# Optimization experiments

Measured on AMD Instinct MI355X. Metric: run time of the kernel, lower is better.

The kernel has to match this reference:

```python
import jax, jax.numpy as jnp
import numpy as np

N = 100000
E = 800000


def sage_conv(h, src, dst, W_l, W_r, b):
    # PyG SAGEConv (mean aggr): lin_l(mean_{j in N(i)} h_j) + lin_r(h_i) + bias
    deg = jax.ops.segment_sum(jnp.ones((src.shape[0],), h.dtype), dst, num_segments=N)
    agg = jax.ops.segment_sum(h[src], dst, num_segments=N)  # [N, d]
    agg = agg / jnp.maximum(deg, 1.0)[:, None]
    return agg @ W_l + h @ W_r + b


def gcn_conv(h, src, dst, W, b):
    # PyG GCNConv with added self-loops and symmetric normalization
    xw = h @ W  # [N, out]
    deg = jax.ops.segment_sum(jnp.ones((src.shape[0],), h.dtype), dst, num_segments=N) + 1.0
    dinv = jax.lax.rsqrt(deg)
    coef = dinv[src] * dinv[dst]  # [E]
    out = jax.ops.segment_sum(xw[src] * coef[:, None], dst, num_segments=N)
    out = out + xw * (1.0 / deg)[:, None]  # self-loop term: dinv[i]*dinv[i]
    return out + b


def fit_and_add(x, h):
    # initial_residual: zero-pad x along feature dim to h's width, then add
    d_in, d_out = x.shape[1], h.shape[1]
    if d_in < d_out:
        x = jnp.pad(x, ((0, 0), (0, d_out - d_in)))
    return x + h


def setup_inputs() -> dict:
    key = jax.random.key(0)
    ks = jax.random.split(key, 12)
    s = lambda d: 1.0 / np.sqrt(d)
    x = jax.random.normal(ks[0], (N, 128), jnp.float32)
    edge_index = jax.random.randint(ks[1], (2, E), 0, N, jnp.int32)
    return {
        "x": x,
        "edge_index": edge_index,
        "W1_l": jax.random.normal(ks[2], (128, 256), jnp.float32) * s(128),
        "W1_r": jax.random.normal(ks[3], (128, 256), jnp.float32) * s(128),
        "b1": jnp.zeros((256,), jnp.float32),
        "W2_l": jax.random.normal(ks[4], (256, 256), jnp.float32) * s(256),
        "W2_r": jax.random.normal(ks[5], (256, 256), jnp.float32) * s(256),
        "b2": jnp.zeros((256,), jnp.float32),
        "Wr": jax.random.normal(ks[6], (128, 256), jnp.float32) * s(128),
        "br": jnp.zeros((256,), jnp.float32),
        "Wmu": jax.random.normal(ks[7], (256, 64), jnp.float32) * s(256),
        "bmu": jnp.zeros((64,), jnp.float32),
        "Wls": jax.random.normal(ks[8], (256, 64), jnp.float32) * s(256),
        "bls": jnp.zeros((64,), jnp.float32),
    }


def reference(x, edge_index, W1_l, W1_r, b1, W2_l, W2_r, b2, Wr, br, Wmu, bmu, Wls, bls):
    src, dst = edge_index[0], edge_index[1]
    h = jax.nn.relu(sage_conv(x, src, dst, W1_l, W1_r, b1))
    h = fit_and_add(x, h)
    h = jax.nn.relu(sage_conv(h, src, dst, W2_l, W2_r, b2))
    h = h + (x @ Wr + br)
    mu = gcn_conv(h, src, dst, Wmu, bmu)
    logstd = gcn_conv(h, src, dst, Wls, bls)
    return mu, logstd
```

## Files before the change

### kernel.cpp

```cpp
#include <hip/hip_runtime.h>
#include <hip/hip_bf16.h>

#define NN 100000
#define EE 800000
#define MPAD 100096
#define MT64 1564
#define MT128 782

typedef __attribute__((ext_vector_type(4))) float f32x4;
typedef __attribute__((ext_vector_type(8))) short s16x8;

__device__ __forceinline__ float bfu(unsigned short u) {
    union { unsigned i; float f; } x; x.i = ((unsigned)u) << 16; return x.f;
}
__device__ __forceinline__ unsigned short fbf(float f) {
    union { float f; unsigned i; } x; x.f = f;
    unsigned r = x.i + (((x.i >> 16) & 1u) + 0x7fffu);
    return (unsigned short)(r >> 16);
}
__device__ __forceinline__ uint4 pack8(const float* a) {
    uint4 o;
    o.x = (unsigned)fbf(a[0]) | ((unsigned)fbf(a[1]) << 16);
    o.y = (unsigned)fbf(a[2]) | ((unsigned)fbf(a[3]) << 16);
    o.z = (unsigned)fbf(a[4]) | ((unsigned)fbf(a[5]) << 16);
    o.w = (unsigned)fbf(a[6]) | ((unsigned)fbf(a[7]) << 16);
    return o;
}
__device__ __forceinline__ void acc8(float* a, uint4 v) {
    a[0] += bfu((unsigned short)v.x); a[1] += bfu((unsigned short)(v.x >> 16));
    a[2] += bfu((unsigned short)v.y); a[3] += bfu((unsigned short)(v.y >> 16));
    a[4] += bfu((unsigned short)v.z); a[5] += bfu((unsigned short)(v.z >> 16));
    a[6] += bfu((unsigned short)v.w); a[7] += bfu((unsigned short)(v.w >> 16));
}
__device__ __forceinline__ void load_lds16(const void* g, void* l) {
    __builtin_amdgcn_global_load_lds((const __attribute__((address_space(1))) void*)g,
                                     (__attribute__((address_space(3))) void*)l, 16, 0, 0);
}


__global__ void hist_k(const int* __restrict__ ei, int* __restrict__ counts) {
    int e = blockIdx.x * 256 + threadIdx.x;
    if (e < EE) atomicAdd(&counts[ei[EE + e]], 1);
}

__global__ void scan1_k(const int* __restrict__ counts, int* __restrict__ rp, int* __restrict__ bsum) {
    __shared__ int lds[256];
    int b = blockIdx.x, t = threadIdx.x;
    int base = b * 1024 + t * 4;
    int v[4]; int s = 0;
#pragma unroll
    for (int j = 0; j < 4; ++j) { v[j] = (base + j < NN) ? counts[base + j] : 0; s += v[j]; }
    lds[t] = s; __syncthreads();
    for (int off = 1; off < 256; off <<= 1) {
        int x = (t >= off) ? lds[t - off] : 0;
        __syncthreads();
        lds[t] += x;
        __syncthreads();
    }
    int run = lds[t] - s;
    if (t == 255) bsum[b] = lds[255];
#pragma unroll
    for (int j = 0; j < 4; ++j) { if (base + j < NN) rp[base + j] = run; run += v[j]; }
}

__global__ void scan2_k(int* __restrict__ bsum, int nb) {
    int l = threadIdx.x;
    int v0 = (l < nb) ? bsum[l] : 0;
    int v1 = (64 + l < nb) ? bsum[64 + l] : 0;
    int s0 = v0, s1 = v1;
    for (int off = 1; off < 64; off <<= 1) {
        int t0 = __shfl_up(s0, off); if (l >= off) s0 += t0;
        int t1 = __shfl_up(s1, off); if (l >= off) s1 += t1;
    }
    int tot0 = __shfl(s0, 63);
    if (l < nb) bsum[l] = s0 - v0;
    if (64 + l < nb) bsum[64 + l] = tot0 + s1 - v1;
}

__global__ void scan3_k(int* __restrict__ rp, const int* __restrict__ bsum,
                        int* __restrict__ counts, float* __restrict__ dinv) {
    int i = blockIdx.x * 256 + threadIdx.x;
    if (i == 0) rp[NN] = EE;
    if (i < NN) {
        int v = rp[i] + bsum[i >> 10];
        int deg = counts[i];
        rp[i] = v;
        counts[i] = v;
        dinv[i] = rsqrtf((float)deg + 1.0f);
    }
}

__global__ void fill_k(const int* __restrict__ ei, int* __restrict__ fill, int* __restrict__ esrc) {
    int e = blockIdx.x * 256 + threadIdx.x;
    if (e < EE) {
        int d = ei[EE + e];
        int slot = atomicAdd(&fill[d], 1);
        esrc[slot] = ei[e];
    }
}


__global__ void xcvt_k(const float* __restrict__ x, __hip_bfloat16* __restrict__ A1) {
    int idx = blockIdx.x * 256 + threadIdx.x;
    if (idx < NN * 32) {
        int row = idx >> 5; int c4 = (idx & 31) * 4;
        float4 v = *(const float4*)(x + (size_t)row * 128 + c4);
        ushort4 o; o.x = fbf(v.x); o.y = fbf(v.y); o.z = fbf(v.z); o.w = fbf(v.w);
        *(ushort4*)((unsigned short*)A1 + (size_t)row * 256 + 128 + c4) = o;
    }
}

__global__ void wprep_k(const float* __restrict__ W1l, const float* __restrict__ W1r,
                        const float* __restrict__ W2l, const float* __restrict__ W2r,
                        const float* __restrict__ Wr,  const float* __restrict__ Wmu,
                        const float* __restrict__ Wls,
                        unsigned short* __restrict__ B1T, unsigned short* __restrict__ B2T,
                        unsigned short* __restrict__ B3T) {
    int idx = blockIdx.x * 256 + threadIdx.x;
    if (idx < 65536) {
        int n = idx >> 8, k = idx & 255;
        float v = (k < 128) ? W1l[k * 256 + n] : W1r[(k - 128) * 256 + n];
        B1T[idx] = fbf(v);
    } else if (idx < 229376) {
        int j = idx - 65536;
        int n = j / 640, k = j - n * 640;
        float v = (k < 256) ? W2l[k * 256 + n]
                : (k < 512) ? W2r[(k - 256) * 256 + n]
                            : Wr[(k - 512) * 256 + n];
        B2T[j] = fbf(v);
    } else if (idx < 262144) {
        int j = idx - 229376;
        int n = j >> 8, k = j & 255;
        float v = (n < 64) ? Wmu[k * 64 + n] : Wls[k * 64 + (n - 64)];
        B3T[j] = fbf(v);
    }
}


__global__ __launch_bounds__(256) void agg1_k(const int* __restrict__ rp, const int* __restrict__ esrc,
                                              __hip_bfloat16* __restrict__ A1) {
    int wid = threadIdx.x >> 6, lane = threadIdx.x & 63;
    int node = blockIdx.x * 4 + wid;
    if (node >= NN) return;
    int e0 = rp[node], e1 = rp[node + 1];
    int sg = lane >> 4, lc = lane & 15;
    const unsigned short* X = (const unsigned short*)A1;
    float a[8] = {};
    for (int e = e0 + sg; e < e1; e += 4) {
        int s = esrc[e];
        uint4 v = *(const uint4*)(X + (size_t)s * 256 + 128 + lc * 8);
        acc8(a, v);
    }
#pragma unroll
    for (int k = 0; k < 8; ++k) {
        a[k] += __shfl_xor(a[k], 16);
        a[k] += __shfl_xor(a[k], 32);
    }
    int deg = e1 - e0;
    float sc = 1.0f / (float)(deg > 1 ? deg : 1);
    if (lane < 16) {
#pragma unroll
        for (int k = 0; k < 8; ++k) a[k] *= sc;
        *(uint4*)((unsigned short*)A1 + (size_t)node * 256 + lane * 8) = pack8(a);
    }
}

__global__ __launch_bounds__(256) void agg2_k(const int* __restrict__ rp, const int* __restrict__ esrc,
                                              const __hip_bfloat16* __restrict__ H1,
                                              __hip_bfloat16* __restrict__ AGG2) {
    int wid = threadIdx.x >> 6, lane = threadIdx.x & 63;
    int node = blockIdx.x * 4 + wid;
    if (node >= NN) return;
    int e0 = rp[node], e1 = rp[node + 1];
    int sg = lane >> 5, lc = lane & 31;
    const unsigned short* H = (const unsigned short*)H1;
    float a[8] = {};
    for (int e = e0 + sg; e < e1; e += 2) {
        int s = esrc[e];
        uint4 v = *(const uint4*)(H + (size_t)s * 256 + lc * 8);
        acc8(a, v);
    }
#pragma unroll
    for (int k = 0; k < 8; ++k) a[k] += __shfl_xor(a[k], 32);
    int deg = e1 - e0;
    float sc = 1.0f / (float)(deg > 1 ? deg : 1);
    if (lane < 32) {
#pragma unroll
        for (int k = 0; k < 8; ++k) a[k] *= sc;
        *(uint4*)((unsigned short*)AGG2 + (size_t)node * 256 + lane * 8) = pack8(a);
    }
}

__global__ __launch_bounds__(256) void gcnagg_k(const int* __restrict__ rp, const int* __restrict__ esrc,
                                                const __hip_bfloat16* __restrict__ XWS,
                                                const float* __restrict__ dinv,
                                                const float* __restrict__ bmu, const float* __restrict__ bls,
                                                float* __restrict__ out) {
    int wid = threadIdx.x >> 6, lane = threadIdx.x & 63;
    int node = blockIdx.x * 4 + wid;
    if (node >= NN) return;
    int e0 = rp[node], e1 = rp[node + 1];
    int sg = lane >> 4, lc = lane & 15;
    const unsigned short* W = (const unsigned short*)XWS;
    float a[8] = {};
    if (sg == 0) {
        uint4 v = *(const uint4*)(W + (size_t)node * 128 + lc * 8);
        acc8(a, v);
    }
    for (int e = e0 + sg; e < e1; e += 4) {
        int s = esrc[e];
        uint4 v = *(const uint4*)(W + (size_t)s * 128 + lc * 8);
        acc8(a, v);
    }
#pragma unroll
    for (int k = 0; k < 8; ++k) {
        a[k] += __shfl_xor(a[k], 16);
        a[k] += __shfl_xor(a[k], 32);
    }
    if (lane < 16) {
        float di = dinv[node];
        int col = lane * 8;
        float o[8];
        if (col < 64) {
#pragma unroll
            for (int k = 0; k < 8; ++k) o[k] = di * a[k] + bmu[col + k];
            *(float4*)(out + (size_t)node * 64 + col) = make_float4(o[0], o[1], o[2], o[3]);
            *(float4*)(out + (size_t)node * 64 + col + 4) = make_float4(o[4], o[5], o[6], o[7]);
        } else {
#pragma unroll
            for (int k = 0; k < 8; ++k) o[k] = di * a[k] + bls[col - 64 + k];
            *(float4*)(out + (size_t)NN * 64 + (size_t)node * 64 + (col - 64)) = make_float4(o[0], o[1], o[2], o[3]);
            *(float4*)(out + (size_t)NN * 64 + (size_t)node * 64 + (col - 60)) = make_float4(o[4], o[5], o[6], o[7]);
        }
    }
}


#define STAGE_T(SRC, LDST, STRIDE, ROWBASE, KOFF, NCH)                                              \
    _Pragma("unroll")                                                                               \
    for (int c_ = 0; c_ < NCH; ++c_) {                                                              \
        int off_ = (c_ * 256 + t) * 16;                                                             \
        int row_ = off_ >> 7;                                                                       \
        int cc_  = (off_ >> 4) & 7;                                                                 \
        int gcb_ = ((cc_ ^ (row_ & 7)) << 4);                                                       \
        int wb_ = (c_ * 256 + (t & ~63)) * 16;                                                      \
        load_lds16((const char*)(SRC) + ((size_t)((ROWBASE) + row_) * (STRIDE) + (KOFF)) * 2 + gcb_,\
                   (char*)(LDST) + wb_);                                                            \
    }

#define COMPUTE_STEP(ACC)                                                                          \
    _Pragma("unroll")                                                                              \
    for (int ks = 0; ks < 2; ++ks) {                                                               \
        int sc_ = (((ks << 2) + (lane >> 4)) ^ (lane & 7)) << 3;                                   \
        s16x8 afr[4], bfr[4];                                                                      \
        _Pragma("unroll")                                                                          \
        for (int i = 0; i < 4; ++i) {                                                              \
            afr[i] = *(const s16x8*)&lA[(wr * 64 + i * 16 + (lane & 15)) * 64 + sc_];              \
            bfr[i] = *(const s16x8*)&lB[(wc * 64 + i * 16 + (lane & 15)) * 64 + sc_];              \
        }                                                                                          \
        _Pragma("unroll")                                                                          \
        for (int i = 0; i < 4; ++i)                                                                \
            _Pragma("unroll")                                                                      \
            for (int j = 0; j < 4; ++j)                                                            \
                ACC[i][j] = __builtin_amdgcn_mfma_f32_16x16x32_bf16(afr[i], bfr[j], ACC[i][j], 0, 0, 0); \
    }

__global__ __launch_bounds__(256) void gemm1_k(const __hip_bfloat16* __restrict__ A1,
                                               const __hip_bfloat16* __restrict__ B1T,
                                               const float* __restrict__ b1,
                                               const float* __restrict__ x,
                                               __hip_bfloat16* __restrict__ H1) {
    __shared__ __hip_bfloat16 lA[64 * 64];
    __shared__ __hip_bfloat16 lB[256 * 64];
    const int bm = blockIdx.x;
    const int t = threadIdx.x, lane = t & 63;
    const int wr = 0, wc = t >> 6;
    const int r0 = bm * 64;
    f32x4 acc[4][4] = {};
    for (int kt = 0; kt < 4; ++kt) {
        STAGE_T(A1, lA, 256, r0, kt * 64, 2);
        STAGE_T(B1T, lB, 256, 0, kt * 64, 8);
        __syncthreads();
        COMPUTE_STEP(acc);
        __syncthreads();
    }
    const int row0 = r0, col0 = wc * 64;
    unsigned short* Hs = (unsigned short*)H1;
#pragma unroll
    for (int i = 0; i < 4; ++i)
#pragma unroll
        for (int j = 0; j < 4; ++j) {
            int col = col0 + j * 16 + (lane & 15);
#pragma unroll
            for (int r = 0; r < 4; ++r) {
                int row = row0 + i * 16 + (lane >> 4) * 4 + r;
                float v = acc[i][j][r] + b1[col];
                v = fmaxf(v, 0.0f);
                if (col < 128 && row < NN) v += x[(size_t)row * 128 + col];
                Hs[(size_t)row * 256 + col] = fbf(v);
            }
        }
}

__global__ __launch_bounds__(256) void gemm2_k(const __hip_bfloat16* __restrict__ AGG2,
                                               const __hip_bfloat16* __restrict__ H1,
                                               const __hip_bfloat16* __restrict__ A1,
                                               const __hip_bfloat16* __restrict__ B2T,
                                               const float* __restrict__ b2,
                                               const float* __restrict__ br,
                                               __hip_bfloat16* __restrict__ H2) {
    __shared__ __hip_bfloat16 lA[64 * 64];
    __shared__ __hip_bfloat16 lB[256 * 64];
    const int bm = blockIdx.x;
    const int t = threadIdx.x, lane = t & 63;
    const int wr = 0, wc = t >> 6;
    const int r0 = bm * 64;
    f32x4 accA[4][4] = {};
    f32x4 accB[4][4] = {};
    for (int kt = 0; kt < 8; ++kt) {
        const __hip_bfloat16* Ab = (kt < 4) ? AGG2 : H1;
        int ko = (kt < 4) ? kt * 64 : (kt - 4) * 64;
        STAGE_T(Ab, lA, 256, r0, ko, 2);
        STAGE_T(B2T, lB, 640, 0, kt * 64, 8);
        __syncthreads();
        COMPUTE_STEP(accA);
        __syncthreads();
    }
    for (int kt = 8; kt < 10; ++kt) {
        STAGE_T(A1, lA, 256, r0, 128 + (kt - 8) * 64, 2);
        STAGE_T(B2T, lB, 640, 0, kt * 64, 8);
        __syncthreads();
        COMPUTE_STEP(accB);
        __syncthreads();
    }
    const int row0 = r0, col0 = wc * 64;
    unsigned short* Hs = (unsigned short*)H2;
#pragma unroll
    for (int i = 0; i < 4; ++i)
#pragma unroll
        for (int j = 0; j < 4; ++j) {
            int col = col0 + j * 16 + (lane & 15);
#pragma unroll
            for (int r = 0; r < 4; ++r) {
                int row = row0 + i * 16 + (lane >> 4) * 4 + r;
                float v = fmaxf(accA[i][j][r] + b2[col], 0.0f) + accB[i][j][r] + br[col];
                Hs[(size_t)row * 256 + col] = fbf(v);
            }
        }
}

__global__ __launch_bounds__(256) void gemm3_k(const __hip_bfloat16* __restrict__ H2,
                                               const __hip_bfloat16* __restrict__ B3T,
                                               const float* __restrict__ dinv,
                                               __hip_bfloat16* __restrict__ XWS) {
    __shared__ __hip_bfloat16 lA[128 * 64];
    __shared__ __hip_bfloat16 lB[128 * 64];
    const int bm = blockIdx.x;
    const int t = threadIdx.x, lane = t & 63, wid = t >> 6;
    const int wr = wid >> 1, wc = wid & 1;
    const int r0 = bm * 128;
    f32x4 acc[4][4] = {};
    for (int kt = 0; kt < 4; ++kt) {
        STAGE_T(H2, lA, 256, r0, kt * 64, 4);
        STAGE_T(B3T, lB, 256, 0, kt * 64, 4);
        __syncthreads();
        COMPUTE_STEP(acc);
        __syncthreads();
    }
    const int row0 = r0 + wr * 64, col0 = wc * 64;
    unsigned short* Ws = (unsigned short*)XWS;
#pragma unroll
    for (int i = 0; i < 4; ++i)
#pragma unroll
        for (int j = 0; j < 4; ++j) {
            int col = col0 + j * 16 + (lane & 15);
#pragma unroll
            for (int r = 0; r < 4; ++r) {
                int row = row0 + i * 16 + (lane >> 4) * 4 + r;
                float di = (row < NN) ? dinv[row] : 0.0f;
                Ws[(size_t)row * 128 + col] = fbf(acc[i][j][r] * di);
            }
        }
}


extern "C" void kernel_launch(void* const* d_in, const int* in_sizes, int n_in,
                              void* d_out, int out_size, void* d_ws, size_t ws_size,
                              hipStream_t stream) {
    const float* x   = (const float*)d_in[0];
    const int*   ei  = (const int*)d_in[1];
    const float* W1l = (const float*)d_in[2];
    const float* W1r = (const float*)d_in[3];
    const float* b1  = (const float*)d_in[4];
    const float* W2l = (const float*)d_in[5];
    const float* W2r = (const float*)d_in[6];
    const float* b2  = (const float*)d_in[7];
    const float* Wr  = (const float*)d_in[8];
    const float* br  = (const float*)d_in[9];
    const float* Wmu = (const float*)d_in[10];
    const float* bmu = (const float*)d_in[11];
    const float* Wls = (const float*)d_in[12];
    const float* bls = (const float*)d_in[13];
    float* out = (float*)d_out;

    char* w = (char*)d_ws;
    size_t o = 0;
    int* counts = (int*)(w + o);           o += 400128;
    int* rp     = (int*)(w + o);           o += 400128;
    int* bsum   = (int*)(w + o);           o += 1024;
    int* esrc   = (int*)(w + o);           o += 3200000;
    float* dinv = (float*)(w + o);         o += 400128;
    unsigned short* B1T = (unsigned short*)(w + o); o += 131072;
    unsigned short* B2T = (unsigned short*)(w + o); o += 327680;
    unsigned short* B3T = (unsigned short*)(w + o); o += 65536;
    __hip_bfloat16* A1   = (__hip_bfloat16*)(w + o); o += (size_t)MPAD * 256 * 2;
    __hip_bfloat16* H1   = (__hip_bfloat16*)(w + o); o += (size_t)MPAD * 256 * 2;
    __hip_bfloat16* AGG2 = (__hip_bfloat16*)(w + o); o += (size_t)MPAD * 256 * 2;
    __hip_bfloat16* H2   = (__hip_bfloat16*)(w + o); o += (size_t)MPAD * 256 * 2;
    __hip_bfloat16* XWS  = AGG2;
    (void)ws_size; (void)in_sizes; (void)n_in; (void)out_size;

    hipMemsetAsync(counts, 0, NN * 4, stream);

    hist_k<<<EE / 256, 256, 0, stream>>>(ei, counts);
    scan1_k<<<98, 256, 0, stream>>>(counts, rp, bsum);
    scan2_k<<<1, 64, 0, stream>>>(bsum, 98);
    scan3_k<<<391, 256, 0, stream>>>(rp, bsum, counts, dinv);
    fill_k<<<EE / 256, 256, 0, stream>>>(ei, counts, esrc);

    xcvt_k<<<NN * 32 / 256, 256, 0, stream>>>(x, A1);
    wprep_k<<<1024, 256, 0, stream>>>(W1l, W1r, W2l, W2r, Wr, Wmu, Wls, B1T, B2T, B3T);

    agg1_k<<<NN / 4, 256, 0, stream>>>(rp, esrc, A1);
    gemm1_k<<<MT64, 256, 0, stream>>>(A1, (const __hip_bfloat16*)B1T, b1, x, H1);
    agg2_k<<<NN / 4, 256, 0, stream>>>(rp, esrc, H1, AGG2);
    gemm2_k<<<MT64, 256, 0, stream>>>(AGG2, H1, A1, (const __hip_bfloat16*)B2T, b2, br, H2);
    gemm3_k<<<MT128, 256, 0, stream>>>(H2, (const __hip_bfloat16*)B3T, dinv, XWS);
    gcnagg_k<<<NN / 4, 256, 0, stream>>>(rp, esrc, XWS, dinv, bmu, bls, out);
}
```

Baseline: 534.4 us.

## Double-buffer LDS in GEMMs and unroll gather loops with dual accumulators

The three GEMM kernels now keep two LDS buffers and prefetch the next K-tile while the current one is computed, which drops one barrier per iteration. gemm2 merges its two loops into one pipelined loop. The aggregation kernels process two edges per iteration with separate accumulators so more gather loads are in flight. gemm1 reads the residual from the bf16 copy of x in A1 instead of the fp32 x, which cuts traffic but slightly lowers precision. Doubling LDS per block (about 80KB in gemm1/gemm2) may reduce occupancy.

```diff
diff --git a/kernel.cpp b/kernel.cpp
--- a/kernel.cpp
+++ b/kernel.cpp
@@ -145,14 +145,21 @@
     int e0 = rp[node], e1 = rp[node + 1];
     int sg = lane >> 4, lc = lane & 15;
     const unsigned short* X = (const unsigned short*)A1;
-    float a[8] = {};
-    for (int e = e0 + sg; e < e1; e += 4) {
-        int s = esrc[e];
-        uint4 v = *(const uint4*)(X + (size_t)s * 256 + 128 + lc * 8);
+    float a[8] = {}, b[8] = {};
+    int e = e0 + sg;
+    for (; e + 4 < e1; e += 8) {
+        int s0 = esrc[e], s1 = esrc[e + 4];
+        uint4 v0 = *(const uint4*)(X + (size_t)s0 * 256 + 128 + lc * 8);
+        uint4 v1 = *(const uint4*)(X + (size_t)s1 * 256 + 128 + lc * 8);
+        acc8(a, v0); acc8(b, v1);
+    }
+    if (e < e1) {
+        uint4 v = *(const uint4*)(X + (size_t)esrc[e] * 256 + 128 + lc * 8);
         acc8(a, v);
     }
 #pragma unroll
     for (int k = 0; k < 8; ++k) {
+        a[k] += b[k];
         a[k] += __shfl_xor(a[k], 16);
         a[k] += __shfl_xor(a[k], 32);
     }
@@ -174,14 +181,23 @@
     int e0 = rp[node], e1 = rp[node + 1];
     int sg = lane >> 5, lc = lane & 31;
     const unsigned short* H = (const unsigned short*)H1;
-    float a[8] = {};
-    for (int e = e0 + sg; e < e1; e += 2) {
-        int s = esrc[e];
-        uint4 v = *(const uint4*)(H + (size_t)s * 256 + lc * 8);
+    float a[8] = {}, b[8] = {};
+    int e = e0 + sg;
+    for (; e + 2 < e1; e += 4) {
+        int s0 = esrc[e], s1 = esrc[e + 2];
+        uint4 v0 = *(const uint4*)(H + (size_t)s0 * 256 + lc * 8);
+        uint4 v1 = *(const uint4*)(H + (size_t)s1 * 256 + lc * 8);
+        acc8(a, v0); acc8(b, v1);
+    }
+    if (e < e1) {
+        uint4 v = *(const uint4*)(H + (size_t)esrc[e] * 256 + lc * 8);
         acc8(a, v);
     }
 #pragma unroll
-    for (int k = 0; k < 8; ++k) a[k] += __shfl_xor(a[k], 32);
+    for (int k = 0; k < 8; ++k) {
+        a[k] += b[k];
+        a[k] += __shfl_xor(a[k], 32);
+    }
     int deg = e1 - e0;
     float sc = 1.0f / (float)(deg > 1 ? deg : 1);
     if (lane < 32) {
@@ -202,18 +218,25 @@
     int e0 = rp[node], e1 = rp[node + 1];
     int sg = lane >> 4, lc = lane & 15;
     const unsigned short* W = (const unsigned short*)XWS;
-    float a[8] = {};
+    float a[8] = {}, b[8] = {};
     if (sg == 0) {
         uint4 v = *(const uint4*)(W + (size_t)node * 128 + lc * 8);
         acc8(a, v);
     }
-    for (int e = e0 + sg; e < e1; e += 4) {
-        int s = esrc[e];
-        uint4 v = *(const uint4*)(W + (size_t)s * 128 + lc * 8);
+    int e = e0 + sg;
+    for (; e + 4 < e1; e += 8) {
+        int s0 = esrc[e], s1 = esrc[e + 4];
+        uint4 v0 = *(const uint4*)(W + (size_t)s0 * 128 + lc * 8);
+        uint4 v1 = *(const uint4*)(W + (size_t)s1 * 128 + lc * 8);
+        acc8(a, v0); acc8(b, v1);
+    }
+    if (e < e1) {
+        uint4 v = *(const uint4*)(W + (size_t)esrc[e] * 128 + lc * 8);
         acc8(a, v);
     }
 #pragma unroll
     for (int k = 0; k < 8; ++k) {
+        a[k] += b[k];
         a[k] += __shfl_xor(a[k], 16);
         a[k] += __shfl_xor(a[k], 32);
     }
@@ -248,15 +271,15 @@
                    (char*)(LDST) + wb_);                                                            \
     }
 
-#define COMPUTE_STEP(ACC)                                                                          \
+#define COMPUTE_STEP(ACC, PA, PB)                                                                  \
     _Pragma("unroll")                                                                              \
     for (int ks = 0; ks < 2; ++ks) {                                                               \
         int sc_ = (((ks << 2) + (lane >> 4)) ^ (lane & 7)) << 3;                                   \
         s16x8 afr[4], bfr[4];                                                                      \
         _Pragma("unroll")                                                                          \
         for (int i = 0; i < 4; ++i) {                                                              \
-            afr[i] = *(const s16x8*)&lA[(wr * 64 + i * 16 + (lane & 15)) * 64 + sc_];              \
-            bfr[i] = *(const s16x8*)&lB[(wc * 64 + i * 16 + (lane & 15)) * 64 + sc_];              \
+            afr[i] = *(const s16x8*)&(PA)[(wr * 64 + i * 16 + (lane & 15)) * 64 + sc_];            \
+            bfr[i] = *(const s16x8*)&(PB)[(wc * 64 + i * 16 + (lane & 15)) * 64 + sc_];            \
         }                                                                                          \
         _Pragma("unroll")                                                                          \
         for (int i = 0; i < 4; ++i)                                                                \
@@ -268,24 +291,30 @@
 __global__ __launch_bounds__(256) void gemm1_k(const __hip_bfloat16* __restrict__ A1,
                                                const __hip_bfloat16* __restrict__ B1T,
                                                const float* __restrict__ b1,
-                                               const float* __restrict__ x,
                                                __hip_bfloat16* __restrict__ H1) {
-    __shared__ __hip_bfloat16 lA[64 * 64];
-    __shared__ __hip_bfloat16 lB[256 * 64];
+    __shared__ __hip_bfloat16 lA[2][64 * 64];
+    __shared__ __hip_bfloat16 lB[2][256 * 64];
     const int bm = blockIdx.x;
     const int t = threadIdx.x, lane = t & 63;
     const int wr = 0, wc = t >> 6;
     const int r0 = bm * 64;
     f32x4 acc[4][4] = {};
+    STAGE_T(A1, lA[0], 256, r0, 0, 2);
+    STAGE_T(B1T, lB[0], 256, 0, 0, 8);
+    __syncthreads();
+    int cur = 0;
     for (int kt = 0; kt < 4; ++kt) {
-        STAGE_T(A1, lA, 256, r0, kt * 64, 2);
-        STAGE_T(B1T, lB, 256, 0, kt * 64, 8);
+        if (kt < 3) {
+            STAGE_T(A1, lA[cur ^ 1], 256, r0, (kt + 1) * 64, 2);
+            STAGE_T(B1T, lB[cur ^ 1], 256, 0, (kt + 1) * 64, 8);
+        }
+        COMPUTE_STEP(acc, lA[cur], lB[cur]);
         __syncthreads();
-        COMPUTE_STEP(acc);
-        __syncthreads();
+        cur ^= 1;
     }
     const int row0 = r0, col0 = wc * 64;
     unsigned short* Hs = (unsigned short*)H1;
+    const unsigned short* Xb = (const unsigned short*)A1;
 #pragma unroll
     for (int i = 0; i < 4; ++i)
 #pragma unroll
@@ -296,7 +325,7 @@
                 int row = row0 + i * 16 + (lane >> 4) * 4 + r;
                 float v = acc[i][j][r] + b1[col];
                 v = fmaxf(v, 0.0f);
-                if (col < 128 && row < NN) v += x[(size_t)row * 128 + col];
+                if (col < 128) v += bfu(Xb[(size_t)row * 256 + 128 + col]);
                 Hs[(size_t)row * 256 + col] = fbf(v);
             }
         }
@@ -309,29 +338,33 @@
                                                const float* __restrict__ b2,
                                                const float* __restrict__ br,
                                                __hip_bfloat16* __restrict__ H2) {
-    __shared__ __hip_bfloat16 lA[64 * 64];
-    __shared__ __hip_bfloat16 lB[256 * 64];
+    __shared__ __hip_bfloat16 lA[2][64 * 64];
+    __shared__ __hip_bfloat16 lB[2][256 * 64];
     const int bm = blockIdx.x;
     const int t = threadIdx.x, lane = t & 63;
     const int wr = 0, wc = t >> 6;
     const int r0 = bm * 64;
     f32x4 accA[4][4] = {};
     f32x4 accB[4][4] = {};
-    for (int kt = 0; kt < 8; ++kt) {
-        const __hip_bfloat16* Ab = (kt < 4) ? AGG2 : H1;
-        int ko = (kt < 4) ? kt * 64 : (kt - 4) * 64;
-        STAGE_T(Ab, lA, 256, r0, ko, 2);
-        STAGE_T(B2T, lB, 640, 0, kt * 64, 8);
+    STAGE_T(AGG2, lA[0], 256, r0, 0, 2);
+    STAGE_T(B2T, lB[0], 640, 0, 0, 8);
+    __syncthreads();
+    int cur = 0;
+    for (int kt = 0; kt < 10; ++kt) {
+        if (kt < 9) {
+            int kn = kt + 1;
+            const __hip_bfloat16* Ab = (kn < 4) ? AGG2 : (kn < 8 ? H1 : A1);
+            int ko = (kn < 4) ? kn * 64 : (kn < 8 ? (kn - 4) * 64 : 128 + (kn - 8) * 64);
+            STAGE_T(Ab, lA[cur ^ 1], 256, r0, ko, 2);
+            STAGE_T(B2T, lB[cur ^ 1], 640, 0, kn * 64, 8);
+        }
+        if (kt < 8) {
+            COMPUTE_STEP(accA, lA[cur], lB[cur]);
+        } else {
+            COMPUTE_STEP(accB, lA[cur], lB[cur]);
+        }
         __syncthreads();
-        COMPUTE_STEP(accA);
-        __syncthreads();
-    }
-    for (int kt = 8; kt < 10; ++kt) {
-        STAGE_T(A1, lA, 256, r0, 128 + (kt - 8) * 64, 2);
-        STAGE_T(B2T, lB, 640, 0, kt * 64, 8);
-        __syncthreads();
-        COMPUTE_STEP(accB);
-        __syncthreads();
+        cur ^= 1;
     }
     const int row0 = r0, col0 = wc * 64;
     unsigned short* Hs = (unsigned short*)H2;
@@ -353,19 +386,25 @@
                                                const __hip_bfloat16* __restrict__ B3T,
                                                const float* __restrict__ dinv,
                                                __hip_bfloat16* __restrict__ XWS) {
-    __shared__ __hip_bfloat16 lA[128 * 64];
-    __shared__ __hip_bfloat16 lB[128 * 64];
+    __shared__ __hip_bfloat16 lA[2][128 * 64];
+    __shared__ __hip_bfloat16 lB[2][128 * 64];
     const int bm = blockIdx.x;
     const int t = threadIdx.x, lane = t & 63, wid = t >> 6;
     const int wr = wid >> 1, wc = wid & 1;
     const int r0 = bm * 128;
     f32x4 acc[4][4] = {};
+    STAGE_T(H2, lA[0], 256, r0, 0, 4);
+    STAGE_T(B3T, lB[0], 256, 0, 0, 4);
+    __syncthreads();
+    int cur = 0;
     for (int kt = 0; kt < 4; ++kt) {
-        STAGE_T(H2, lA, 256, r0, kt * 64, 4);
-        STAGE_T(B3T, lB, 256, 0, kt * 64, 4);
+        if (kt < 3) {
+            STAGE_T(H2, lA[cur ^ 1], 256, r0, (kt + 1) * 64, 4);
+            STAGE_T(B3T, lB[cur ^ 1], 256, 0, (kt + 1) * 64, 4);
+        }
+        COMPUTE_STEP(acc, lA[cur], lB[cur]);
         __syncthreads();
-        COMPUTE_STEP(acc);
-        __syncthreads();
+        cur ^= 1;
     }
     const int row0 = r0 + wr * 64, col0 = wc * 64;
     unsigned short* Ws = (unsigned short*)XWS;
@@ -432,7 +471,7 @@
     wprep_k<<<1024, 256, 0, stream>>>(W1l, W1r, W2l, W2r, Wr, Wmu, Wls, B1T, B2T, B3T);
 
     agg1_k<<<NN / 4, 256, 0, stream>>>(rp, esrc, A1);
-    gemm1_k<<<MT64, 256, 0, stream>>>(A1, (const __hip_bfloat16*)B1T, b1, x, H1);
+    gemm1_k<<<MT64, 256, 0, stream>>>(A1, (const __hip_bfloat16*)B1T, b1, H1);
     agg2_k<<<NN / 4, 256, 0, stream>>>(rp, esrc, H1, AGG2);
     gemm2_k<<<MT64, 256, 0, stream>>>(AGG2, H1, A1, (const __hip_bfloat16*)B2T, b2, br, H2);
     gemm3_k<<<MT128, 256, 0, stream>>>(H2, (const __hip_bfloat16*)B3T, dinv, XWS);
```

Measured after the change: 523.9 us. -2.0%, faster.
